# Kernel tuning notes

Hardware: AMD Instinct MI355X
Metric: run time of the kernel (lower is better)

The kernel has to match this reference:

```python
import jax, jax.numpy as jnp
import numpy as np

SIZE = 4096
LOG_N = 12  # log2(SIZE)
BATCH = 8192


def setup_inputs() -> dict:
    key = jax.random.key(0)
    k1, k2 = jax.random.split(key)
    x = jax.random.normal(k1, (BATCH, SIZE), dtype=jnp.float32)
    # one (SIZE//2, 2, 2) real twiddle bank per layer, stacked; init ~ randn/sqrt(2)
    twiddles = jax.random.normal(k2, (LOG_N, SIZE // 2, 2, 2), dtype=jnp.float32) / np.sqrt(2.0).astype(np.float32)
    return {"x": x, "twiddles": twiddles}


def _butterfly_forward(x, twiddles):
    # x: [B, n]; twiddles: [log_n, n//2, 2, 2]
    B, n = x.shape
    log_n = twiddles.shape[0]
    out = x
    for layer in range(log_n):
        stride = 2 ** (log_n - layer - 1)
        n_blocks = n // (2 * stride)
        # block b, offset i: top = out[:, b, 0, i], bot = out[:, b, 1, i]
        xr = out.reshape(B, n_blocks, 2, stride)
        top = xr[:, :, 0, :]  # [B, nb, stride]
        bot = xr[:, :, 1, :]
        # twiddle_idx = b*stride + i  ->  reshape to (nb, stride, 2, 2)
        w = twiddles[layer].reshape(n_blocks, stride, 2, 2)
        new_top = w[None, :, :, 0, 0] * top + w[None, :, :, 0, 1] * bot
        new_bot = w[None, :, :, 1, 0] * top + w[None, :, :, 1, 1] * bot
        out = jnp.stack([new_top, new_bot], axis=2).reshape(B, n)
    return out


def reference(x, twiddles):
    return _butterfly_forward(x, twiddles)
```

## Files before the change

### kernel.cpp

```cpp
#include <hip/hip_runtime.h>

#define ROWS 4
#define N 4096
#define BATCH 8192
#define S_AB 264
#define ARENA 4224
#define NWS_F4 (8 * 2048)

typedef float v4f __attribute__((ext_vector_type(4)));

__device__ __forceinline__ void half_layer(float (&v)[ROWS][16],
                                           const float4 (&s)[4],
                                           const int bit, const int pcb) {
    const int d = 1 << bit;
    #pragma unroll
    for (int i = 0; i < 4; ++i) {
        const int pc = pcb + i;
        const int lo = ((pc >> bit) << (bit + 1)) | (pc & (d - 1));
        const int hi = lo + d;
        #pragma unroll
        for (int r = 0; r < ROWS; ++r) {
            const float top = v[r][lo], bot = v[r][hi];
            v[r][lo] = s[i].x * top + s[i].y * bot;
            v[r][hi] = s[i].z * top + s[i].w * bot;
        }
    }
}

__global__ __launch_bounds__(256)
void permute_tw_kernel(const float* __restrict__ tw, float4* __restrict__ nws) {
    const int i = blockIdx.x * 256 + threadIdx.x;
    const int s  = i >> 11;
    const int j  = i & 2047;
    const int pc = j >> 8;
    const int a  = (j >> 4) & 15;
    const int cb = j & 15;
    const float4* tw4 = (const float4*)tw;
    const int src = (s < 4) ? (a * 128 + pc * 16 + cb)
                            : (a * 128 + cb * 8 + pc);
    nws[i] = tw4[(4 + s) * 2048 + src];
}

__global__ __launch_bounds__(256, 2)
void butterfly_kernel(const float* __restrict__ x,
                      const float* __restrict__ tw,
                      const float4* __restrict__ nws,
                      float* __restrict__ out) {
    __shared__ float lds[2 * ARENA];
    float* bufA = lds;
    float* bufB = lds + ARENA;
    const int t   = threadIdx.x;
    const int thi = t >> 4;
    const int tlo = t & 15;
    const int row0 = blockIdx.x * ROWS;
    const float4* tw4 = (const float4*)tw;

    auto ldA = [&](int l, int pcb, float4 (&s)[4]) {
        #pragma unroll
        for (int i = 0; i < 4; ++i) s[i] = tw4[l * 2048 + (pcb + i) * 256 + t];
    };
    auto ldN = [&](int l, int pcb, float4 (&s)[4]) {
        #pragma unroll
        for (int i = 0; i < 4; ++i) s[i] = nws[(l - 4) * 2048 + (pcb + i) * 256 + t];
    };

    float v[ROWS][16];
    float4 S0[4], S1[4], S2[4];

    {
        const float* r0 = x + (size_t)(row0 + 0) * N + 4 * t;
        const float* r1 = x + (size_t)(row0 + 1) * N + 4 * t;
        const float* r2 = x + (size_t)(row0 + 2) * N + 4 * t;
        const float* r3 = x + (size_t)(row0 + 3) * N + 4 * t;
        v4f t0[4], t1[4];
        #pragma unroll
        for (int i = 0; i < 4; ++i) t0[i] = *(const v4f*)(r0 + i * 1024);
        #pragma unroll
        for (int i = 0; i < 4; ++i) t1[i] = *(const v4f*)(r1 + i * 1024);
        #pragma unroll
        for (int i = 0; i < 4; ++i) *(v4f*)(bufA + i * 1024 + 4 * t) = t0[i];
        #pragma unroll
        for (int i = 0; i < 4; ++i) *(v4f*)(bufB + i * 1024 + 4 * t) = t1[i];
        #pragma unroll
        for (int i = 0; i < 4; ++i) t0[i] = *(const v4f*)(r2 + i * 1024);
        #pragma unroll
        for (int i = 0; i < 4; ++i) t1[i] = *(const v4f*)(r3 + i * 1024);
        __syncthreads();
        #pragma unroll
        for (int a = 0; a < 16; ++a) v[0][a] = bufA[a * 256 + t];
        #pragma unroll
        for (int a = 0; a < 16; ++a) v[1][a] = bufB[a * 256 + t];
        __syncthreads();
        #pragma unroll
        for (int i = 0; i < 4; ++i) *(v4f*)(bufA + i * 1024 + 4 * t) = t0[i];
        #pragma unroll
        for (int i = 0; i < 4; ++i) *(v4f*)(bufB + i * 1024 + 4 * t) = t1[i];
        ldA(0, 0, S0);
        ldA(0, 4, S1);
        __syncthreads();
        #pragma unroll
        for (int a = 0; a < 16; ++a) v[2][a] = bufA[a * 256 + t];
        #pragma unroll
        for (int a = 0; a < 16; ++a) v[3][a] = bufB[a * 256 + t];
    }

    ldA(1, 0, S2); half_layer(v, S0, 3, 0); ldA(1, 4, S0); half_layer(v, S1, 3, 4);
    ldA(2, 0, S1); half_layer(v, S2, 2, 0); ldA(2, 4, S2); half_layer(v, S0, 2, 4);
    ldA(3, 0, S0); half_layer(v, S1, 1, 0); ldA(3, 4, S1); half_layer(v, S2, 1, 4);
    ldN(4, 0, S2); half_layer(v, S0, 0, 0); ldN(4, 4, S0); half_layer(v, S1, 0, 4);

    __syncthreads();
    #pragma unroll
    for (int a = 0; a < 16; ++a) bufA[a * S_AB + t] = v[0][a];
    #pragma unroll
    for (int a = 0; a < 16; ++a) bufB[a * S_AB + t] = v[1][a];
    __syncthreads();
    #pragma unroll
    for (int b = 0; b < 16; ++b) v[0][b] = bufA[thi * S_AB + b * 16 + tlo];
    #pragma unroll
    for (int b = 0; b < 16; ++b) v[1][b] = bufB[thi * S_AB + b * 16 + tlo];
    __syncthreads();
    #pragma unroll
    for (int a = 0; a < 16; ++a) bufA[a * S_AB + t] = v[2][a];
    #pragma unroll
    for (int a = 0; a < 16; ++a) bufB[a * S_AB + t] = v[3][a];
    __syncthreads();
    #pragma unroll
    for (int b = 0; b < 16; ++b) v[2][b] = bufA[thi * S_AB + b * 16 + tlo];
    #pragma unroll
    for (int b = 0; b < 16; ++b) v[3][b] = bufB[thi * S_AB + b * 16 + tlo];

    ldN(5, 0, S1); half_layer(v, S2, 3, 0); ldN(5, 4, S2); half_layer(v, S0, 3, 4);
    ldN(6, 0, S0); half_layer(v, S1, 2, 0); ldN(6, 4, S1); half_layer(v, S2, 2, 4);
    ldN(7, 0, S2); half_layer(v, S0, 1, 0); ldN(7, 4, S0); half_layer(v, S1, 1, 4);
    ldN(8, 0, S1); half_layer(v, S2, 0, 0); ldN(8, 4, S2); half_layer(v, S0, 0, 4);

    {
        __syncthreads();
        #pragma unroll
        for (int b = 0; b < 16; ++b) {
            const int coff = 4 * (((tlo >> 2) ^ (b & 3))) + (tlo & 3);
            bufA[thi * S_AB + b * 16 + coff] = v[0][b];
            bufB[thi * S_AB + b * 16 + coff] = v[1][b];
        }
        __syncthreads();
        #pragma unroll
        for (int rr = 0; rr < 2; ++rr) {
            const float* bp = (rr ? bufB : bufA) + thi * S_AB + tlo * 16;
            #pragma unroll
            for (int q = 0; q < 4; ++q) {
                v4f c4 = *(const v4f*)(bp + 4 * (q ^ (tlo & 3)));
                v[rr][4 * q + 0] = c4.x; v[rr][4 * q + 1] = c4.y;
                v[rr][4 * q + 2] = c4.z; v[rr][4 * q + 3] = c4.w;
            }
        }
        __syncthreads();
        #pragma unroll
        for (int b = 0; b < 16; ++b) {
            const int coff = 4 * (((tlo >> 2) ^ (b & 3))) + (tlo & 3);
            bufA[thi * S_AB + b * 16 + coff] = v[2][b];
            bufB[thi * S_AB + b * 16 + coff] = v[3][b];
        }
        __syncthreads();
        #pragma unroll
        for (int rr = 2; rr < 4; ++rr) {
            const float* bp = (rr == 3 ? bufB : bufA) + thi * S_AB + tlo * 16;
            #pragma unroll
            for (int q = 0; q < 4; ++q) {
                v4f c4 = *(const v4f*)(bp + 4 * (q ^ (tlo & 3)));
                v[rr][4 * q + 0] = c4.x; v[rr][4 * q + 1] = c4.y;
                v[rr][4 * q + 2] = c4.z; v[rr][4 * q + 3] = c4.w;
            }
        }
    }

    ldN(9,  0, S0); half_layer(v, S1, 3, 0); ldN(9,  4, S1); half_layer(v, S2, 3, 4);
    ldN(10, 0, S2); half_layer(v, S0, 2, 0); ldN(10, 4, S0); half_layer(v, S1, 2, 4);
    ldN(11, 0, S1); half_layer(v, S2, 1, 0); ldN(11, 4, S2); half_layer(v, S0, 1, 4);
                    half_layer(v, S1, 0, 0);                 half_layer(v, S2, 0, 4);

    {
        v4f* fA = (v4f*)bufA;
        v4f* fB = (v4f*)bufB;
        const int wsel = (t >> 2) & 3;
        __syncthreads();
        #pragma unroll
        for (int h = 0; h < 2; ++h) {
            #pragma unroll
            for (int rr = 0; rr < 2; ++rr) {
                v4f* f = rr ? fB : fA;
                const int r = 2 * h + rr;
                #pragma unroll
                for (int q = 0; q < 4; ++q) {
                    v4f s4;
                    s4.x = v[r][4 * q + 0]; s4.y = v[r][4 * q + 1];
                    s4.z = v[r][4 * q + 2]; s4.w = v[r][4 * q + 3];
                    f[4 * t + (q ^ wsel)] = s4;
                }
            }
            __syncthreads();
            #pragma unroll
            for (int rr = 0; rr < 2; ++rr) {
                v4f* f = rr ? fB : fA;
                const int r = 2 * h + rr;
                float* orow = out + (size_t)(row0 + r) * N;
                #pragma unroll
                for (int k = 0; k < 4; ++k) {
                    const int j = k * 256 + t;
                    v4f s4 = f[(j & ~3) | ((j & 3) ^ ((j >> 4) & 3))];
                    __builtin_nontemporal_store(s4, (v4f*)orow + j);
                }
            }
            if (h == 0) __syncthreads();
        }
    }
}

#define PAD_STRIDE 264
#define BUF_WORDS (16 * PAD_STRIDE)

__device__ __forceinline__ void layer16(float (&v)[4][16], const float4 (&w)[8], const int bit) {
    const int d = 1 << bit;
    #pragma unroll
    for (int pc = 0; pc < 8; ++pc) {
        const int lo = ((pc >> bit) << (bit + 1)) | (pc & (d - 1));
        const int hi = lo + d;
        #pragma unroll
        for (int r = 0; r < 4; ++r) {
            const float top = v[r][lo], bot = v[r][hi];
            v[r][lo] = w[pc].x * top + w[pc].y * bot;
            v[r][hi] = w[pc].z * top + w[pc].w * bot;
        }
    }
}

__global__ __launch_bounds__(256, 3)
void butterfly_kernel_fb(const float* __restrict__ x,
                         const float* __restrict__ tw,
                         float* __restrict__ out) {
    __shared__ float lds[BUF_WORDS];
    const int t = threadIdx.x;
    const int thi = t >> 4, tlo = t & 15;
    const int row0 = blockIdx.x * 4;
    const float4* tw4 = (const float4*)tw;
    float v[4][16];
    #pragma unroll
    for (int r = 0; r < 4; ++r) {
        const float* xr = x + (size_t)(row0 + r) * N + t;
        #pragma unroll
        for (int a = 0; a < 16; ++a) v[r][a] = __builtin_nontemporal_load(xr + a * 256);
    }
    #pragma unroll
    for (int l = 0; l < 4; ++l) {
        float4 w[8];
        #pragma unroll
        for (int pc = 0; pc < 8; ++pc) w[pc] = tw4[l * 2048 + pc * 256 + t];
        layer16(v, w, 3 - l);
    }
    #pragma unroll
    for (int r = 0; r < 4; ++r) {
        #pragma unroll
        for (int a = 0; a < 16; ++a) lds[a * PAD_STRIDE + t] = v[r][a];
        __syncthreads();
        #pragma unroll
        for (int b = 0; b < 16; ++b) v[r][b] = lds[thi * PAD_STRIDE + b * 16 + tlo];
        __syncthreads();
    }
    #pragma unroll
    for (int l = 4; l < 8; ++l) {
        float4 w[8];
        #pragma unroll
        for (int pc = 0; pc < 8; ++pc) w[pc] = tw4[l * 2048 + thi * 128 + pc * 16 + tlo];
        layer16(v, w, 3 - (l - 4));
    }
    #pragma unroll
    for (int r = 0; r < 4; ++r) {
        #pragma unroll
        for (int b = 0; b < 16; ++b) lds[thi * PAD_STRIDE + b * 16 + tlo] = v[r][b];
        __syncthreads();
        const float* bp = &lds[thi * PAD_STRIDE + tlo * 16];
        #pragma unroll
        for (int q = 0; q < 4; ++q) {
            v4f c4 = *(const v4f*)(bp + 4 * q);
            v[r][4 * q + 0] = c4.x; v[r][4 * q + 1] = c4.y;
            v[r][4 * q + 2] = c4.z; v[r][4 * q + 3] = c4.w;
        }
        if (r != 3) __syncthreads();
    }
    #pragma unroll
    for (int l = 8; l < 12; ++l) {
        float4 w[8];
        #pragma unroll
        for (int pc = 0; pc < 8; ++pc) w[pc] = tw4[l * 2048 + thi * 128 + tlo * 8 + pc];
        layer16(v, w, 3 - (l - 8));
    }
    #pragma unroll
    for (int r = 0; r < 4; ++r) {
        float* orow = out + (size_t)(row0 + r) * N + 16 * t;
        #pragma unroll
        for (int q = 0; q < 4; ++q) {
            v4f s4;
            s4.x = v[r][4 * q + 0]; s4.y = v[r][4 * q + 1];
            s4.z = v[r][4 * q + 2]; s4.w = v[r][4 * q + 3];
            *(v4f*)(orow + 4 * q) = s4;
        }
    }
}

extern "C" void kernel_launch(void* const* d_in, const int* in_sizes, int n_in,
                              void* d_out, int out_size, void* d_ws, size_t ws_size,
                              hipStream_t stream) {
    const float* x  = (const float*)d_in[0];
    const float* tw = (const float*)d_in[1];
    float* out      = (float*)d_out;
    dim3 block(256);
    if (ws_size >= (size_t)NWS_F4 * 16u) {
        float4* nws = (float4*)d_ws;
        hipLaunchKernelGGL(permute_tw_kernel, dim3(64), block, 0, stream, tw, nws);
        hipLaunchKernelGGL(butterfly_kernel, dim3(BATCH / ROWS), block, 0, stream,
                           x, tw, nws, out);
    } else {
        hipLaunchKernelGGL(butterfly_kernel_fb, dim3(BATCH / 4), block, 0, stream,
                           x, tw, out);
    }
}
```

Baseline: 64.83 us.

## Halve rows per block and raise occupancy with single twiddle buffer

Each block now processes 2 rows instead of 4, and launch bounds move from 2 to 4 blocks per SU. The triple-buffered twiddle register prefetch is replaced with a single buffer that is loaded right before each half-layer. The goal is to cut register pressure and the number of LDS round-trips per block so more waves can hide latency. In exchange, each twiddle load is amortised over half as many rows and is no longer software-prefetched, and the grid size must double for the kernel to stay correct.

Result: slower. 77.47 us (+19.5%).

```diff
diff --git a/kernel.cpp b/kernel.cpp
--- a/kernel.cpp
+++ b/kernel.cpp
@@ -1,6 +1,6 @@
 #include <hip/hip_runtime.h>
 
-#define ROWS 4
+#define ROWS 2
 #define N 4096
 #define BATCH 8192
 #define S_AB 264
@@ -41,7 +41,7 @@
     nws[i] = tw4[(4 + s) * 2048 + src];
 }
 
-__global__ __launch_bounds__(256, 2)
+__global__ __launch_bounds__(256, 4)
 void butterfly_kernel(const float* __restrict__ x,
                       const float* __restrict__ tw,
                       const float4* __restrict__ nws,
@@ -65,13 +65,11 @@
     };
 
     float v[ROWS][16];
-    float4 S0[4], S1[4], S2[4];
+    float4 S[4];
 
     {
         const float* r0 = x + (size_t)(row0 + 0) * N + 4 * t;
         const float* r1 = x + (size_t)(row0 + 1) * N + 4 * t;
-        const float* r2 = x + (size_t)(row0 + 2) * N + 4 * t;
-        const float* r3 = x + (size_t)(row0 + 3) * N + 4 * t;
         v4f t0[4], t1[4];
         #pragma unroll
         for (int i = 0; i < 4; ++i) t0[i] = *(const v4f*)(r0 + i * 1024);
@@ -81,33 +79,18 @@
         for (int i = 0; i < 4; ++i) *(v4f*)(bufA + i * 1024 + 4 * t) = t0[i];
         #pragma unroll
         for (int i = 0; i < 4; ++i) *(v4f*)(bufB + i * 1024 + 4 * t) = t1[i];
-        #pragma unroll
-        for (int i = 0; i < 4; ++i) t0[i] = *(const v4f*)(r2 + i * 1024);
-        #pragma unroll
-        for (int i = 0; i < 4; ++i) t1[i] = *(const v4f*)(r3 + i * 1024);
         __syncthreads();
         #pragma unroll
         for (int a = 0; a < 16; ++a) v[0][a] = bufA[a * 256 + t];
         #pragma unroll
         for (int a = 0; a < 16; ++a) v[1][a] = bufB[a * 256 + t];
-        __syncthreads();
-        #pragma unroll
-        for (int i = 0; i < 4; ++i) *(v4f*)(bufA + i * 1024 + 4 * t) = t0[i];
-        #pragma unroll
-        for (int i = 0; i < 4; ++i) *(v4f*)(bufB + i * 1024 + 4 * t) = t1[i];
-        ldA(0, 0, S0);
-        ldA(0, 4, S1);
-        __syncthreads();
-        #pragma unroll
-        for (int a = 0; a < 16; ++a) v[2][a] = bufA[a * 256 + t];
-        #pragma unroll
-        for (int a = 0; a < 16; ++a) v[3][a] = bufB[a * 256 + t];
-    }
-
-    ldA(1, 0, S2); half_layer(v, S0, 3, 0); ldA(1, 4, S0); half_layer(v, S1, 3, 4);
-    ldA(2, 0, S1); half_layer(v, S2, 2, 0); ldA(2, 4, S2); half_layer(v, S0, 2, 4);
-    ldA(3, 0, S0); half_layer(v, S1, 1, 0); ldA(3, 4, S1); half_layer(v, S2, 1, 4);
-    ldN(4, 0, S2); half_layer(v, S0, 0, 0); ldN(4, 4, S0); half_layer(v, S1, 0, 4);
+    }
+
+    #pragma unroll
+    for (int l = 0; l < 4; ++l) {
+        ldA(l, 0, S); half_layer(v, S, 3 - l, 0);
+        ldA(l, 4, S); half_layer(v, S, 3 - l, 4);
+    }
 
     __syncthreads();
     #pragma unroll
@@ -119,65 +102,37 @@
     for (int b = 0; b < 16; ++b) v[0][b] = bufA[thi * S_AB + b * 16 + tlo];
     #pragma unroll
     for (int b = 0; b < 16; ++b) v[1][b] = bufB[thi * S_AB + b * 16 + tlo];
-    __syncthreads();
-    #pragma unroll
-    for (int a = 0; a < 16; ++a) bufA[a * S_AB + t] = v[2][a];
-    #pragma unroll
-    for (int a = 0; a < 16; ++a) bufB[a * S_AB + t] = v[3][a];
-    __syncthreads();
-    #pragma unroll
-    for (int b = 0; b < 16; ++b) v[2][b] = bufA[thi * S_AB + b * 16 + tlo];
-    #pragma unroll
-    for (int b = 0; b < 16; ++b) v[3][b] = bufB[thi * S_AB + b * 16 + tlo];
-
-    ldN(5, 0, S1); half_layer(v, S2, 3, 0); ldN(5, 4, S2); half_layer(v, S0, 3, 4);
-    ldN(6, 0, S0); half_layer(v, S1, 2, 0); ldN(6, 4, S1); half_layer(v, S2, 2, 4);
-    ldN(7, 0, S2); half_layer(v, S0, 1, 0); ldN(7, 4, S0); half_layer(v, S1, 1, 4);
-    ldN(8, 0, S1); half_layer(v, S2, 0, 0); ldN(8, 4, S2); half_layer(v, S0, 0, 4);
-
-    {
-        __syncthreads();
-        #pragma unroll
-        for (int b = 0; b < 16; ++b) {
-            const int coff = 4 * (((tlo >> 2) ^ (b & 3))) + (tlo & 3);
-            bufA[thi * S_AB + b * 16 + coff] = v[0][b];
-            bufB[thi * S_AB + b * 16 + coff] = v[1][b];
-        }
-        __syncthreads();
-        #pragma unroll
-        for (int rr = 0; rr < 2; ++rr) {
-            const float* bp = (rr ? bufB : bufA) + thi * S_AB + tlo * 16;
-            #pragma unroll
-            for (int q = 0; q < 4; ++q) {
-                v4f c4 = *(const v4f*)(bp + 4 * (q ^ (tlo & 3)));
-                v[rr][4 * q + 0] = c4.x; v[rr][4 * q + 1] = c4.y;
-                v[rr][4 * q + 2] = c4.z; v[rr][4 * q + 3] = c4.w;
-            }
-        }
-        __syncthreads();
-        #pragma unroll
-        for (int b = 0; b < 16; ++b) {
-            const int coff = 4 * (((tlo >> 2) ^ (b & 3))) + (tlo & 3);
-            bufA[thi * S_AB + b * 16 + coff] = v[2][b];
-            bufB[thi * S_AB + b * 16 + coff] = v[3][b];
-        }
-        __syncthreads();
-        #pragma unroll
-        for (int rr = 2; rr < 4; ++rr) {
-            const float* bp = (rr == 3 ? bufB : bufA) + thi * S_AB + tlo * 16;
-            #pragma unroll
-            for (int q = 0; q < 4; ++q) {
-                v4f c4 = *(const v4f*)(bp + 4 * (q ^ (tlo & 3)));
-                v[rr][4 * q + 0] = c4.x; v[rr][4 * q + 1] = c4.y;
-                v[rr][4 * q + 2] = c4.z; v[rr][4 * q + 3] = c4.w;
-            }
-        }
-    }
-
-    ldN(9,  0, S0); half_layer(v, S1, 3, 0); ldN(9,  4, S1); half_layer(v, S2, 3, 4);
-    ldN(10, 0, S2); half_layer(v, S0, 2, 0); ldN(10, 4, S0); half_layer(v, S1, 2, 4);
-    ldN(11, 0, S1); half_layer(v, S2, 1, 0); ldN(11, 4, S2); half_layer(v, S0, 1, 4);
-                    half_layer(v, S1, 0, 0);                 half_layer(v, S2, 0, 4);
+
+    #pragma unroll
+    for (int l = 4; l < 8; ++l) {
+        ldN(l, 0, S); half_layer(v, S, 3 - (l - 4), 0);
+        ldN(l, 4, S); half_layer(v, S, 3 - (l - 4), 4);
+    }
+
+    __syncthreads();
+    #pragma unroll
+    for (int b = 0; b < 16; ++b) {
+        const int coff = 4 * (((tlo >> 2) ^ (b & 3))) + (tlo & 3);
+        bufA[thi * S_AB + b * 16 + coff] = v[0][b];
+        bufB[thi * S_AB + b * 16 + coff] = v[1][b];
+    }
+    __syncthreads();
+    #pragma unroll
+    for (int rr = 0; rr < 2; ++rr) {
+        const float* bp = (rr ? bufB : bufA) + thi * S_AB + tlo * 16;
+        #pragma unroll
+        for (int q = 0; q < 4; ++q) {
+            v4f c4 = *(const v4f*)(bp + 4 * (q ^ (tlo & 3)));
+            v[rr][4 * q + 0] = c4.x; v[rr][4 * q + 1] = c4.y;
+            v[rr][4 * q + 2] = c4.z; v[rr][4 * q + 3] = c4.w;
+        }
+    }
+
+    #pragma unroll
+    for (int l = 8; l < 12; ++l) {
+        ldN(l, 0, S); half_layer(v, S, 3 - (l - 8), 0);
+        ldN(l, 4, S); half_layer(v, S, 3 - (l - 8), 4);
+    }
 
     {
         v4f* fA = (v4f*)bufA;
@@ -185,33 +140,27 @@
         const int wsel = (t >> 2) & 3;
         __syncthreads();
         #pragma unroll
-        for (int h = 0; h < 2; ++h) {
+        for (int rr = 0; rr < 2; ++rr) {
+            v4f* f = rr ? fB : fA;
             #pragma unroll
-            for (int rr = 0; rr < 2; ++rr) {
-                v4f* f = rr ? fB : fA;
-                const int r = 2 * h + rr;
-                #pragma unroll
-                for (int q = 0; q < 4; ++q) {
-                    v4f s4;
-                    s4.x = v[r][4 * q + 0]; s4.y = v[r][4 * q + 1];
-                    s4.z = v[r][4 * q + 2]; s4.w = v[r][4 * q + 3];
-                    f[4 * t + (q ^ wsel)] = s4;
-                }
+            for (int q = 0; q < 4; ++q) {
+                v4f s4;
+                s4.x = v[rr][4 * q + 0]; s4.y = v[rr][4 * q + 1];
+                s4.z = v[rr][4 * q + 2]; s4.w = v[rr][4 * q + 3];
+                f[4 * t + (q ^ wsel)] = s4;
             }
-            __syncthreads();
+        }
+        __syncthreads();
+        #pragma unroll
+        for (int rr = 0; rr < 2; ++rr) {
+            v4f* f = rr ? fB : fA;
+            float* orow = out + (size_t)(row0 + rr) * N;
             #pragma unroll
-            for (int rr = 0; rr < 2; ++rr) {
-                v4f* f = rr ? fB : fA;
-                const int r = 2 * h + rr;
-                float* orow = out + (size_t)(row0 + r) * N;
-                #pragma unroll
-                for (int k = 0; k < 4; ++k) {
-                    const int j = k * 256 + t;
-                    v4f s4 = f[(j & ~3) | ((j & 3) ^ ((j >> 4) & 3))];
-                    __builtin_nontemporal_store(s4, (v4f*)orow + j);
-                }
+            for (int k = 0; k < 4; ++k) {
+                const int j = k * 256 + t;
+                v4f s4 = f[(j & ~3) | ((j & 3) ^ ((j >> 4) & 3))];
+                __builtin_nontemporal_store(s4, (v4f*)orow + j);
             }
-            if (h == 0) __syncthreads();
         }
     }
 }
```
